# Kernel tuning notes

Hardware: AMD Instinct MI355X
Metric: run time of the kernel (lower is better)

## Reference

```python
import jax, jax.numpy as jnp
import numpy as np

B, S, E, H = 8, 1024, 1024, 16
D = E // H  # head_dim = 64


def setup_inputs() -> dict:
    key = jax.random.key(0)
    ks = jax.random.split(key, 10)
    def lin(k):
        kw, kb = jax.random.split(k)
        lim = 1.0 / np.sqrt(E)
        W = jax.random.uniform(kw, (E, E), jnp.float32, -lim, lim)
        b = jax.random.uniform(kb, (E,), jnp.float32, -lim, lim)
        return W, b
    Wq, bq = lin(ks[0]); Wk, bk = lin(ks[1]); Wv, bv = lin(ks[2]); Wo, bo = lin(ks[3])
    ent = jax.random.normal(ks[4], (H, H), jnp.float32)
    x = jax.random.normal(ks[5], (B, S, E), jnp.float32)
    mask = jnp.ones((B, 1, S, S), jnp.int32)
    return {"x": x, "mask": mask, "Wq": Wq, "bq": bq, "Wk": Wk, "bk": bk,
            "Wv": Wv, "bv": bv, "Wo": Wo, "bo": bo, "ent": ent}


def reference(x, mask, Wq, bq, Wk, bk, Wv, bv, Wo, bo, ent):
    Bs, Sl, Ed = x.shape
    def heads(W, b):
        return (x @ W.T + b).reshape(Bs, Sl, H, D).transpose(0, 2, 1, 3)  # [B,H,S,D]
    q, k, v = heads(Wq, bq), heads(Wk, bk), heads(Wv, bv)
    scores = jnp.einsum('bhqd,bhkd->bhqk', q, k) / np.sqrt(D)  # [B,H,S,S]
    Em = jax.nn.softmax(ent, axis=-1)  # [H,H]
    scores = jnp.einsum('bhqk,hg->bgqk', scores, Em)  # cross-head entanglement mix
    scores = jnp.where(mask == 0, jnp.float32(-1e9), scores)
    attn = jax.nn.softmax(scores, axis=-1)
    out = jnp.einsum('bhqk,bhkd->bhqd', attn, v)
    out = out.transpose(0, 2, 1, 3).reshape(Bs, Sl, Ed)
    return out @ Wo.T + bo
```

## Files before the change

### kernel.cpp

```cpp
#include <hip/hip_runtime.h>

#define DEVINL static __device__ __forceinline__

typedef __attribute__((ext_vector_type(4)))  float f32x4;
typedef __attribute__((ext_vector_type(16))) float f32x16;
typedef __attribute__((ext_vector_type(4)))  float float4_t;
typedef __attribute__((ext_vector_type(8)))  short short8;
typedef __attribute__((ext_vector_type(4)))  short short4v;
typedef __attribute__((ext_vector_type(4)))  int   int4v;

DEVINL unsigned short f2bf(float f){
  union { float f; unsigned int u; } x; x.f = f;
  return (unsigned short)((x.u + 0x7fffu + ((x.u >> 16) & 1u)) >> 16);
}
DEVINL float bf2f(unsigned short h){
  union { unsigned int u; float f; } x; x.u = ((unsigned int)h) << 16;
  return x.f;
}
DEVINL f32x4 zero4(){ f32x4 z; z[0]=0.f; z[1]=0.f; z[2]=0.f; z[3]=0.f; return z; }
DEVINL f32x16 zero16(){ f32x16 z;
#pragma unroll
  for (int e=0;e<16;++e) z[e]=0.f;
  return z; }

#define GLL16(gp, lp) __builtin_amdgcn_global_load_lds( \
    (const __attribute__((address_space(1))) void*)(gp), \
    (__attribute__((address_space(3))) void*)(lp), 16, 0, 0)

__global__ __launch_bounds__(256) void cast_f32_bf16(const float* __restrict__ src,
                                                     unsigned short* __restrict__ dst, int n8){
  int i = blockIdx.x * 256 + threadIdx.x;
  if (i >= n8) return;
  const float4_t* s = (const float4_t*)src;
  float4_t a = s[2*i], b = s[2*i+1];
  short8 o;
  o[0]=(short)f2bf(a[0]); o[1]=(short)f2bf(a[1]); o[2]=(short)f2bf(a[2]); o[3]=(short)f2bf(a[3]);
  o[4]=(short)f2bf(b[0]); o[5]=(short)f2bf(b[1]); o[6]=(short)f2bf(b[2]); o[7]=(short)f2bf(b[3]);
  *(short8*)(dst + (size_t)i*8) = o;
}

__global__ __launch_bounds__(256) void prep_em(const float* __restrict__ ent,
                                               unsigned short* __restrict__ EmT){
  int t = threadIdx.x;
  if (t < 16){
    float v[16]; float mx = -3.0e38f;
#pragma unroll
    for (int j=0;j<16;++j){ v[j] = ent[t*16 + j]; mx = fmaxf(mx, v[j]); }
    float s = 0.f;
#pragma unroll
    for (int j=0;j<16;++j){ v[j] = __expf(v[j]-mx); s += v[j]; }
    float inv = (1.f/s) * 0.125f * 1.4426950408889634f;
#pragma unroll
    for (int j=0;j<16;++j) EmT[j*16 + t] = f2bf(v[j]*inv);
  }
  EmT[256 + t] = 0;
}

__global__ __launch_bounds__(256) void prep_maskbits(const int* __restrict__ mask,
                                                     unsigned* __restrict__ mb){
  int id = blockIdx.x * 256 + threadIdx.x;
  const int* src = mask + (size_t)id * 32;
  unsigned word = 0u;
#pragma unroll
  for (int c=0;c<8;++c){
    int4v v = *(const int4v*)(src + c*4);
    word |= (unsigned)(v[0]!=0) << (c*4)
          | (unsigned)(v[1]!=0) << (c*4+1)
          | (unsigned)(v[2]!=0) << (c*4+2)
          | (unsigned)(v[3]!=0) << (c*4+3);
  }
  mb[id] = word;
}

template<int MODE>
__global__ __launch_bounds__(256) void gemm_bt(const unsigned short* __restrict__ A,
                                               const unsigned short* __restrict__ W4,
                                               const float* __restrict__ bias0,
                                               const float* __restrict__ bias1,
                                               const float* __restrict__ bias2,
                                               void* __restrict__ outp){
  __shared__ __align__(16) unsigned short As[4096];
  __shared__ __align__(16) unsigned short Bs[4096];
  const int tid = threadIdx.x;
  const int w = tid >> 6, ln = tid & 63;
  const int wm = w >> 1, wn = w & 1;
  const int lq = ln & 15, lg = ln >> 4;
  const int m0 = blockIdx.y * 128, n0 = blockIdx.x * 128;
  const int z = blockIdx.z;
  const unsigned short* Bt = W4 + (size_t)z * 1048576;
  const float* bias = (z == 0) ? bias0 : ((z == 1) ? bias1 : bias2);

  const unsigned short* Ag = A  + (size_t)(m0 + (tid >> 2)) * 1024 + (tid & 3) * 8;
  const unsigned short* Bg = Bt + (size_t)(n0 + (tid >> 2)) * 1024 + (tid & 3) * 8;
  unsigned short* lA0 = As + w * 512;
  unsigned short* lA1 = As + 2048 + w * 512;
  unsigned short* lB0 = Bs + w * 512;
  unsigned short* lB1 = Bs + 2048 + w * 512;

  f32x4 acc[4][4];
#pragma unroll
  for (int i=0;i<4;++i)
#pragma unroll
    for (int j=0;j<4;++j) acc[i][j] = zero4();

  for (int kb = 0; kb < 32; ++kb){
    const int k0 = kb * 32;
    GLL16(Ag + k0,         lA0);
    GLL16(Ag + k0 + 65536, lA1);
    GLL16(Bg + k0,         lB0);
    GLL16(Bg + k0 + 65536, lB1);
    __syncthreads();
    short8 af[4], bf_[4];
#pragma unroll
    for (int i=0;i<4;++i) af[i]  = *(const short8*)(As + (wm*64 + i*16 + lq)*32 + lg*8);
#pragma unroll
    for (int j=0;j<4;++j) bf_[j] = *(const short8*)(Bs + (wn*64 + j*16 + lq)*32 + lg*8);
#pragma unroll
    for (int i=0;i<4;++i)
#pragma unroll
      for (int j=0;j<4;++j)
        acc[i][j] = __builtin_amdgcn_mfma_f32_16x16x32_bf16(af[i], bf_[j], acc[i][j], 0, 0, 0);
    __syncthreads();
  }

  const int mrow = m0 + wm*64, ncol = n0 + wn*64;
  float bj[4];
#pragma unroll
  for (int j=0;j<4;++j) bj[j] = bias[ncol + j*16 + lq];
#pragma unroll
  for (int i=0;i<4;++i)
#pragma unroll
    for (int j=0;j<4;++j)
#pragma unroll
      for (int r=0;r<4;++r){
        float v = acc[i][j][r] + bj[j];
        int m = mrow + i*16 + lg*4 + r;
        int n = ncol + j*16 + lq;
        if (MODE == 0){
          int bb = m >> 10, sI = m & 1023, h = n >> 6, d = n & 63;
          ((unsigned short*)outp)[(size_t)z*8388608 + (((size_t)bb*16 + h)*1024 + sI)*64 + d] = f2bf(v);
        } else {
          ((float*)outp)[(size_t)m*1024 + n] = v;
        }
      }
}

__global__ __launch_bounds__(256) void transpose_v(const unsigned short* __restrict__ V,
                                                   unsigned short* __restrict__ Vt){
  int idx = blockIdx.x * 256 + threadIdx.x;
  int s8 = idx & 127, d = (idx >> 7) & 63, bh = idx >> 13;
  const unsigned short* src = V + (size_t)bh*65536 + (size_t)s8*8*64 + d;
  short8 o;
#pragma unroll
  for (int j=0;j<8;++j) o[j] = (short)src[(size_t)j*64];
  *(short8*)(Vt + (size_t)bh*65536 + (size_t)d*1024 + (size_t)s8*8) = o;
}

__global__ __launch_bounds__(512,4) void attn_fused(const unsigned short* __restrict__ Q,
    const unsigned short* __restrict__ K, const unsigned short* __restrict__ Vt,
    const unsigned* __restrict__ MB, const unsigned short* __restrict__ EmT,
    unsigned short* __restrict__ AO){
  __shared__ __align__(16) unsigned short sraw[8192];
  __shared__ __align__(16) unsigned short smix[8192];
  const int tid = threadIdx.x;
  const int w = tid >> 6, ln = tid & 63;
  const int lq = ln & 15, lg = ln >> 4;
  const int l5 = ln & 31, h5 = ln >> 5;
  const int bid = blockIdx.x;
  const int bb = bid & 7, q0 = (bid >> 3) * 16;
  const int aQ = w & 3, n0 = w >> 2, g0 = w * 2;

  const unsigned short* Qb = Q  + ((size_t)bb*16 + 4*aQ) * 65536;
  const unsigned short* Kb = K  + ((size_t)bb*16 + 4*aQ) * 65536 + (size_t)(n0*16 + lq)*64 + lg*8;
  const unsigned short* Vb = Vt + ((size_t)bb*16 + g0) * 65536;
  const unsigned* Mw = MB + (size_t)bb*32768 + (size_t)(q0 + lq)*32;

  short8 emA = *(const short8*)(EmT + l5*16 + h5*8);

  short8 qf[4][2];
#pragma unroll
  for (int hh=0; hh<4; ++hh)
#pragma unroll
    for (int ks=0; ks<2; ++ks)
      qf[hh][ks] = *(const short8*)(Qb + (size_t)hh*65536 + (size_t)(q0 + lq)*64 + ks*32 + lg*8);

  f32x4 acco[2][4];
#pragma unroll
  for (int a=0;a<2;++a)
#pragma unroll
    for (int n=0;n<4;++n) acco[a][n] = zero4();
  float mst[2] = {-3.0e38f,-3.0e38f};
  float lst[2] = {0.f,0.f};

  const int kk = n0*16 + lq;

  for (int kt = 0; kt < 32; ++kt){
    const int kb = kt*32;
    f32x4 accs[4];
#pragma unroll
    for (int hh=0; hh<4; ++hh){
      short8 k0 = *(const short8*)(Kb + (size_t)hh*65536 + (size_t)kb*64);
      short8 k1 = *(const short8*)(Kb + (size_t)hh*65536 + (size_t)kb*64 + 32);
      accs[hh] = __builtin_amdgcn_mfma_f32_16x16x32_bf16(qf[hh][0], k0, zero4(), 0,0,0);
      accs[hh] = __builtin_amdgcn_mfma_f32_16x16x32_bf16(qf[hh][1], k1, accs[hh], 0,0,0);
    }
#pragma unroll
    for (int r=0;r<4;++r){
      const int qq = lg*4 + r;
      short4v pk;
      pk[0]=(short)f2bf(accs[0][r]); pk[1]=(short)f2bf(accs[1][r]);
      pk[2]=(short)f2bf(accs[2][r]); pk[3]=(short)f2bf(accs[3][r]);
      const int lin = (qq*32 + kk)*32 + aQ*8;
      const int sw  = (((kk>>2)&1)<<4) | (((qq>>2)&3)<<5);
      *(short4v*)((char*)sraw + (lin ^ sw)) = pk;
    }
    __syncthreads();
#pragma unroll
    for (int t=0;t<2;++t){
      const int qq = w*2 + t;
      const int lin = (qq*32 + l5)*32 + h5*16;
      const int sw  = (((l5>>2)&1)<<4) | (((qq>>2)&3)<<5);
      short8 sfr = *(const short8*)((const char*)sraw + (lin ^ sw));
      f32x16 md = __builtin_amdgcn_mfma_f32_32x32x16_bf16(emA, sfr, zero16(), 0,0,0);
#pragma unroll
      for (int reg=0;reg<8;++reg){
        const int gg = (reg&3) + 8*(reg>>2) + 4*h5;
        int ob = gg*1024 + qq*64 + l5*2;
        ob ^= ((gg>>2)&1)<<6;
        *(short*)((char*)smix + ob) = (short)f2bf(md[reg]);
      }
    }
    __syncthreads();
    const unsigned mw = Mw[kt];
    const unsigned mshift = mw >> (lg*8);
    const int allon = __all((int)((mshift & 0xffu) == 0xffu));
#pragma unroll
    for (int hh=0; hh<2; ++hh){
      const int gg = g0 + hh;
      const int rb = (gg*1024 + lq*64 + lg*16) ^ (((gg>>2)&1)<<6);
      short8 sm8 = *(const short8*)((const char*)smix + rb);
      short8 vfr[4];
#pragma unroll
      for (int n=0;n<4;++n)
        vfr[n] = *(const short8*)(Vb + (size_t)hh*65536 + (size_t)(n*16 + lq)*1024 + kb + lg*8);
      float s[8];
#pragma unroll
      for (int j=0;j<8;++j) s[j] = bf2f((unsigned short)sm8[j]);
      if (!allon){
#pragma unroll
        for (int j=0;j<8;++j) if (!((mshift>>j)&1u)) s[j] = -1.44269504e9f;
      }
      float pm = s[0];
#pragma unroll
      for (int j=1;j<8;++j) pm = fmaxf(pm, s[j]);
      pm = fmaxf(pm, __shfl_xor(pm, 16, 64));
      pm = fmaxf(pm, __shfl_xor(pm, 32, 64));
      const float mo = mst[hh];
      const float mn = fmaxf(mo, pm);
      const float sc = exp2f(mo - mn);
      float p[8]; float ps = 0.f;
#pragma unroll
      for (int j=0;j<8;++j){ p[j] = exp2f(s[j] - mn); ps += p[j]; }
      ps += __shfl_xor(ps, 16, 64);
      ps += __shfl_xor(ps, 32, 64);
      lst[hh] = lst[hh]*sc + ps;
      mst[hh] = mn;
      short8 pa;
#pragma unroll
      for (int j=0;j<8;++j) pa[j] = (short)f2bf(p[j]);
      const float scr0 = __shfl(sc, lg*4 + 0, 64);
      const float scr1 = __shfl(sc, lg*4 + 1, 64);
      const float scr2 = __shfl(sc, lg*4 + 2, 64);
      const float scr3 = __shfl(sc, lg*4 + 3, 64);
#pragma unroll
      for (int n=0;n<4;++n){
        acco[hh][n][0] *= scr0; acco[hh][n][1] *= scr1;
        acco[hh][n][2] *= scr2; acco[hh][n][3] *= scr3;
      }
#pragma unroll
      for (int n=0;n<4;++n)
        acco[hh][n] = __builtin_amdgcn_mfma_f32_16x16x32_bf16(pa, vfr[n], acco[hh][n], 0,0,0);
    }
  }
#pragma unroll
  for (int hh=0; hh<2; ++hh){
    const int gg = g0 + hh;
    const float linv = 1.0f / lst[hh];
    const float l0 = __shfl(linv, lg*4+0, 64), l1 = __shfl(linv, lg*4+1, 64);
    const float l2 = __shfl(linv, lg*4+2, 64), l3 = __shfl(linv, lg*4+3, 64);
#pragma unroll
    for (int n=0;n<4;++n){
      const int e = gg*64 + n*16 + lq;
      const size_t base = ((size_t)bb*1024 + (size_t)(q0 + lg*4))*1024 + e;
      AO[base         ] = f2bf(acco[hh][n][0]*l0);
      AO[base + 1024  ] = f2bf(acco[hh][n][1]*l1);
      AO[base + 2048  ] = f2bf(acco[hh][n][2]*l2);
      AO[base + 3072  ] = f2bf(acco[hh][n][3]*l3);
    }
  }
}

extern "C" void kernel_launch(void* const* d_in, const int* in_sizes, int n_in,
                              void* d_out, int out_size, void* d_ws, size_t ws_size,
                              hipStream_t stream){
  const float* x   = (const float*)d_in[0];
  const int*   msk = (const int*)  d_in[1];
  const float* Wq  = (const float*)d_in[2];
  const float* bq  = (const float*)d_in[3];
  const float* Wk  = (const float*)d_in[4];
  const float* bk  = (const float*)d_in[5];
  const float* Wv  = (const float*)d_in[6];
  const float* bv  = (const float*)d_in[7];
  const float* Wo  = (const float*)d_in[8];
  const float* bo  = (const float*)d_in[9];
  const float* ent = (const float*)d_in[10];

  char* ws = (char*)d_ws;
  unsigned short* xb  = (unsigned short*)(ws);
  unsigned short* Wb  = (unsigned short*)(ws + 16777216);
  unsigned short* qkv = (unsigned short*)(ws + 25165824);
  unsigned short* EmT = (unsigned short*)(ws + 75497472);
  unsigned*       MB  = (unsigned*)     (ws + 75499520);
  unsigned short* Vt  = xb;
  unsigned short* AO  = qkv + (size_t)2*8388608;

  cast_f32_bf16<<<4096, 256, 0, stream>>>(x,  xb,            1048576);
  cast_f32_bf16<<<512,  256, 0, stream>>>(Wq, Wb,            131072);
  cast_f32_bf16<<<512,  256, 0, stream>>>(Wk, Wb + 1048576,  131072);
  cast_f32_bf16<<<512,  256, 0, stream>>>(Wv, Wb + 2097152,  131072);
  cast_f32_bf16<<<512,  256, 0, stream>>>(Wo, Wb + 3145728,  131072);
  prep_em<<<1, 256, 0, stream>>>(ent, EmT);
  prep_maskbits<<<1024, 256, 0, stream>>>(msk, MB);

  gemm_bt<0><<<dim3(8,64,3), 256, 0, stream>>>(xb, Wb, bq, bk, bv, (void*)qkv);
  transpose_v<<<4096, 256, 0, stream>>>(qkv + (size_t)2*8388608, Vt);
  attn_fused<<<512, 512, 0, stream>>>(qkv, qkv + 8388608, Vt, MB, EmT, AO);
  gemm_bt<1><<<dim3(8,64,1), 256, 0, stream>>>(AO, Wb + 3145728, bo, bo, bo, d_out);

  (void)in_sizes; (void)n_in; (void)out_size; (void)ws_size;
}
```

Baseline: 496.8 us.

## Reload Q per tile, transpose PV MFMA, use custom LDS-only barriers in attention

Drops the persistent Q fragment registers and reloads Q from global (cache) each key tile, which lowers register pressure for the 512-thread, 4-wave-per-SIMD launch bound. The PV MFMA operands are swapped so each lane owns one query row, which removes the cross-lane shuffles for the rescale factor and the final normalizer and lets the output be written as packed 32-bit stores. The __syncthreads calls are replaced by a barrier that waits only on LDS counters, so global V and mask loads can stay in flight across it. The costs are extra global and L2 traffic for the repeated Q loads and barrier code that is more fragile.

New measurement: 465.5 us. -6.3%, faster.

```diff
diff --git a/kernel.cpp b/kernel.cpp
--- a/kernel.cpp
+++ b/kernel.cpp
@@ -22,6 +22,14 @@
 #pragma unroll
   for (int e=0;e<16;++e) z[e]=0.f;
   return z; }
+
+#define BARX() do{ \
+  __builtin_amdgcn_sched_barrier(0); \
+  asm volatile("s_waitcnt lgkmcnt(0)" ::: "memory"); \
+  __builtin_amdgcn_sched_barrier(0); \
+  __builtin_amdgcn_s_barrier(); \
+  __builtin_amdgcn_sched_barrier(0); \
+}while(0)
 
 #define GLL16(gp, lp) __builtin_amdgcn_global_load_lds( \
     (const __attribute__((address_space(1))) void*)(gp), \
@@ -170,19 +178,12 @@
   const int bb = bid & 7, q0 = (bid >> 3) * 16;
   const int aQ = w & 3, n0 = w >> 2, g0 = w * 2;
 
-  const unsigned short* Qb = Q  + ((size_t)bb*16 + 4*aQ) * 65536;
+  const unsigned short* Qb = Q  + ((size_t)bb*16 + 4*aQ) * 65536 + (size_t)(q0 + lq)*64 + lg*8;
   const unsigned short* Kb = K  + ((size_t)bb*16 + 4*aQ) * 65536 + (size_t)(n0*16 + lq)*64 + lg*8;
-  const unsigned short* Vb = Vt + ((size_t)bb*16 + g0) * 65536;
-  const unsigned* Mw = MB + (size_t)bb*32768 + (size_t)(q0 + lq)*32;
+  const unsigned short* Vb = Vt + ((size_t)bb*16 + g0) * 65536 + (size_t)lq*1024 + lg*8;
+  const unsigned* Mwp = MB + (size_t)bb*32768 + (size_t)(q0 + lq)*32;
 
   short8 emA = *(const short8*)(EmT + l5*16 + h5*8);
-
-  short8 qf[4][2];
-#pragma unroll
-  for (int hh=0; hh<4; ++hh)
-#pragma unroll
-    for (int ks=0; ks<2; ++ks)
-      qf[hh][ks] = *(const short8*)(Qb + (size_t)hh*65536 + (size_t)(q0 + lq)*64 + ks*32 + lg*8);
 
   f32x4 acco[2][4];
 #pragma unroll
@@ -196,13 +197,16 @@
 
   for (int kt = 0; kt < 32; ++kt){
     const int kb = kt*32;
+    const unsigned mw = Mwp[kt];
     f32x4 accs[4];
 #pragma unroll
     for (int hh=0; hh<4; ++hh){
-      short8 k0 = *(const short8*)(Kb + (size_t)hh*65536 + (size_t)kb*64);
-      short8 k1 = *(const short8*)(Kb + (size_t)hh*65536 + (size_t)kb*64 + 32);
-      accs[hh] = __builtin_amdgcn_mfma_f32_16x16x32_bf16(qf[hh][0], k0, zero4(), 0,0,0);
-      accs[hh] = __builtin_amdgcn_mfma_f32_16x16x32_bf16(qf[hh][1], k1, accs[hh], 0,0,0);
+      short8 q0f = *(const short8*)(Qb + (size_t)hh*65536);
+      short8 q1f = *(const short8*)(Qb + (size_t)hh*65536 + 32);
+      short8 k0f = *(const short8*)(Kb + (size_t)hh*65536 + (size_t)kb*64);
+      short8 k1f = *(const short8*)(Kb + (size_t)hh*65536 + (size_t)kb*64 + 32);
+      accs[hh] = __builtin_amdgcn_mfma_f32_16x16x32_bf16(q0f, k0f, zero4(), 0,0,0);
+      accs[hh] = __builtin_amdgcn_mfma_f32_16x16x32_bf16(q1f, k1f, accs[hh], 0,0,0);
     }
 #pragma unroll
     for (int r=0;r<4;++r){
@@ -214,7 +218,7 @@
       const int sw  = (((kk>>2)&1)<<4) | (((qq>>2)&3)<<5);
       *(short4v*)((char*)sraw + (lin ^ sw)) = pk;
     }
-    __syncthreads();
+    BARX();
 #pragma unroll
     for (int t=0;t<2;++t){
       const int qq = w*2 + t;
@@ -230,37 +234,37 @@
         *(short*)((char*)smix + ob) = (short)f2bf(md[reg]);
       }
     }
-    __syncthreads();
-    const unsigned mw = Mw[kt];
-    const unsigned mshift = mw >> (lg*8);
-    const int allon = __all((int)((mshift & 0xffu) == 0xffu));
+    BARX();
+    const unsigned msh = (mw >> (lg*8)) & 0xffu;
+    const int allon = __all((int)(msh == 0xffu));
 #pragma unroll
     for (int hh=0; hh<2; ++hh){
       const int gg = g0 + hh;
+      short8 vfr[4];
+#pragma unroll
+      for (int n=0;n<4;++n)
+        vfr[n] = *(const short8*)(Vb + (size_t)hh*65536 + (size_t)n*16384 + kb);
       const int rb = (gg*1024 + lq*64 + lg*16) ^ (((gg>>2)&1)<<6);
       short8 sm8 = *(const short8*)((const char*)smix + rb);
-      short8 vfr[4];
-#pragma unroll
-      for (int n=0;n<4;++n)
-        vfr[n] = *(const short8*)(Vb + (size_t)hh*65536 + (size_t)(n*16 + lq)*1024 + kb + lg*8);
       float s[8];
 #pragma unroll
       for (int j=0;j<8;++j) s[j] = bf2f((unsigned short)sm8[j]);
       if (!allon){
 #pragma unroll
-        for (int j=0;j<8;++j) if (!((mshift>>j)&1u)) s[j] = -1.44269504e9f;
+        for (int j=0;j<8;++j) if (!((msh>>j)&1u)) s[j] = -1.44269504e9f;
       }
-      float pm = s[0];
-#pragma unroll
-      for (int j=1;j<8;++j) pm = fmaxf(pm, s[j]);
+      float m01 = fmaxf(s[0],s[1]), m23 = fmaxf(s[2],s[3]);
+      float m45 = fmaxf(s[4],s[5]), m67 = fmaxf(s[6],s[7]);
+      float pm = fmaxf(fmaxf(m01,m23), fmaxf(m45,m67));
       pm = fmaxf(pm, __shfl_xor(pm, 16, 64));
       pm = fmaxf(pm, __shfl_xor(pm, 32, 64));
       const float mo = mst[hh];
       const float mn = fmaxf(mo, pm);
       const float sc = exp2f(mo - mn);
-      float p[8]; float ps = 0.f;
-#pragma unroll
-      for (int j=0;j<8;++j){ p[j] = exp2f(s[j] - mn); ps += p[j]; }
+      float p[8];
+#pragma unroll
+      for (int j=0;j<8;++j) p[j] = exp2f(s[j] - mn);
+      float ps = ((p[0]+p[1]) + (p[2]+p[3])) + ((p[4]+p[5]) + (p[6]+p[7]));
       ps += __shfl_xor(ps, 16, 64);
       ps += __shfl_xor(ps, 32, 64);
       lst[hh] = lst[hh]*sc + ps;
@@ -268,34 +272,26 @@
       short8 pa;
 #pragma unroll
       for (int j=0;j<8;++j) pa[j] = (short)f2bf(p[j]);
-      const float scr0 = __shfl(sc, lg*4 + 0, 64);
-      const float scr1 = __shfl(sc, lg*4 + 1, 64);
-      const float scr2 = __shfl(sc, lg*4 + 2, 64);
-      const float scr3 = __shfl(sc, lg*4 + 3, 64);
 #pragma unroll
       for (int n=0;n<4;++n){
-        acco[hh][n][0] *= scr0; acco[hh][n][1] *= scr1;
-        acco[hh][n][2] *= scr2; acco[hh][n][3] *= scr3;
+        acco[hh][n][0] *= sc; acco[hh][n][1] *= sc;
+        acco[hh][n][2] *= sc; acco[hh][n][3] *= sc;
+        acco[hh][n] = __builtin_amdgcn_mfma_f32_16x16x32_bf16(vfr[n], pa, acco[hh][n], 0,0,0);
       }
-#pragma unroll
-      for (int n=0;n<4;++n)
-        acco[hh][n] = __builtin_amdgcn_mfma_f32_16x16x32_bf16(pa, vfr[n], acco[hh][n], 0,0,0);
     }
   }
 #pragma unroll
   for (int hh=0; hh<2; ++hh){
     const int gg = g0 + hh;
     const float linv = 1.0f / lst[hh];
-    const float l0 = __shfl(linv, lg*4+0, 64), l1 = __shfl(linv, lg*4+1, 64);
-    const float l2 = __shfl(linv, lg*4+2, 64), l3 = __shfl(linv, lg*4+3, 64);
+    const size_t rowb = ((size_t)(bb*1024 + q0 + lq))*2048;
 #pragma unroll
     for (int n=0;n<4;++n){
-      const int e = gg*64 + n*16 + lq;
-      const size_t base = ((size_t)bb*1024 + (size_t)(q0 + lg*4))*1024 + e;
-      AO[base         ] = f2bf(acco[hh][n][0]*l0);
-      AO[base + 1024  ] = f2bf(acco[hh][n][1]*l1);
-      AO[base + 2048  ] = f2bf(acco[hh][n][2]*l2);
-      AO[base + 3072  ] = f2bf(acco[hh][n][3]*l3);
+      unsigned w0 = (unsigned)f2bf(acco[hh][n][0]*linv) | ((unsigned)f2bf(acco[hh][n][1]*linv) << 16);
+      unsigned w1 = (unsigned)f2bf(acco[hh][n][2]*linv) | ((unsigned)f2bf(acco[hh][n][3]*linv) << 16);
+      const int e = gg*64 + n*16 + lg*4;
+      *(unsigned*)((char*)AO + rowb + (size_t)e*2    ) = w0;
+      *(unsigned*)((char*)AO + rowb + (size_t)e*2 + 4) = w1;
     }
   }
 }
```
